# Kernel tuning notes

Measured on AMD Instinct MI355X. Metric: run time of the kernel, lower is better.

## Reference

```python
import jax, jax.numpy as jnp
import numpy as np

NUM_HEADS = 16
ROPE_BASE = 10000.0


def _rope_cos_sin(seq_len, head_dim, dtype):
    inv_freq = 1.0 / (ROPE_BASE ** (jnp.arange(0, head_dim, 2, dtype=jnp.float32) / head_dim))
    t = jnp.arange(seq_len, dtype=jnp.float32)
    freqs = t[:, None] * inv_freq[None, :]          # [S, hd/2]
    emb = jnp.concatenate([freqs, freqs], axis=-1)  # [S, hd]
    return jnp.cos(emb).astype(dtype), jnp.sin(emb).astype(dtype)


def _rotate_half(x):
    x1, x2 = jnp.split(x, 2, axis=-1)
    return jnp.concatenate([-x2, x1], axis=-1)


def setup_inputs() -> dict:
    key = jax.random.key(0)
    ks = jax.random.split(key, 5)
    B, S, D = 2, 2048, 2048
    x = jax.random.normal(ks[0], (B, S, D), dtype=jnp.float32)
    Wq = jax.random.normal(ks[1], (D, D), dtype=jnp.float32) * (D ** -0.5)
    Wk = jax.random.normal(ks[2], (D, D), dtype=jnp.float32) * (D ** -0.5)
    Wv = jax.random.normal(ks[3], (D, D), dtype=jnp.float32) * (D ** -0.5)
    Wo = jax.random.normal(ks[4], (D, D), dtype=jnp.float32) * (D ** -0.5)
    return {"x": x, "Wq": Wq, "Wk": Wk, "Wv": Wv, "Wo": Wo}


def reference(x, Wq, Wk, Wv, Wo):
    B, S, D = x.shape
    H = NUM_HEADS
    hd = D // H
    scale = hd ** -0.5
    # Linear(bias=False): y = x @ W.T ; reshape to [B, H, S, hd]
    def proj(W):
        return jnp.einsum('bsd,ed->bse', x, W).reshape(B, S, H, hd).transpose(0, 2, 1, 3)
    q, k, v = proj(Wq), proj(Wk), proj(Wv)
    cos, sin = _rope_cos_sin(S, hd, x.dtype)  # [S, hd]
    cos = cos[None, None, :, :]
    sin = sin[None, None, :, :]
    q = q * cos + _rotate_half(q) * sin
    k = k * cos + _rotate_half(k) * sin
    scores = jnp.einsum('bhqd,bhkd->bhqk', q, k) * scale  # [B,H,S,S]
    causal = jnp.triu(jnp.ones((S, S), dtype=bool), k=1)
    scores = jnp.where(causal[None, None], jnp.finfo(scores.dtype).min, scores)
    attn = jax.nn.softmax(scores, axis=-1)
    out = jnp.einsum('bhqk,bhkd->bhqd', attn, v)  # [B,H,S,hd]
    out = out.transpose(0, 2, 1, 3).reshape(B, S, D)
    return jnp.einsum('bsd,ed->bse', out, Wo)
```

## Files before the change

### kernel.cpp

```cpp
#include <hip/hip_runtime.h>
#include <hip/hip_bf16.h>
#include <math.h>

typedef __bf16 bf16_t;
typedef __attribute__((ext_vector_type(8))) __bf16 bf16x8;
typedef __attribute__((ext_vector_type(4))) float f32x4;

#define S_LEN 2048
#define DM    2048
#define NH    16
#define HD    128
#define MTOT  4096

__device__ inline float finz(float v) {
    return (v == v && fabsf(v) < 1e30f) ? v : 0.f;
}

__device__ inline void gload_lds16(const bf16_t* g, bf16_t* l) {
    __builtin_amdgcn_global_load_lds(
        (const __attribute__((address_space(1))) void*)g,
        (__attribute__((address_space(3))) void*)l, 16, 0, 0);
}

__global__ __launch_bounds__(256)
void dtype_probe(const unsigned short* __restrict__ p, unsigned int* __restrict__ flag)
{
    __shared__ int tot;
    if (threadIdx.x == 0) tot = 0;
    __syncthreads();
    int weird = 0;
    for (int i = threadIdx.x; i < 4096; i += 256) {
        unsigned short u = p[2*i];
        int e = (u >> 7) & 0xFF;
        if (e >= 0xC8 || (e != 0 && e <= 0x38)) weird++;
    }
    atomicAdd(&tot, weird);
    __syncthreads();
    if (threadIdx.x == 0) *flag = (tot > 512) ? 1u : 0u;
}

__global__ __launch_bounds__(256)
void convert_in(const void* __restrict__ src, bf16_t* __restrict__ dst, int n,
                const unsigned int* __restrict__ flag)
{
    const bool f32 = (*flag != 0);
    int i = (blockIdx.x*256 + threadIdx.x)*4;
    if (i + 3 >= n) return;
    if (f32) {
        const float4 v = *(const float4*)((const float*)src + i);
        dst[i  ] = (bf16_t)v.x; dst[i+1] = (bf16_t)v.y;
        dst[i+2] = (bf16_t)v.z; dst[i+3] = (bf16_t)v.w;
    } else {
        *(uint2*)(dst + i) = *(const uint2*)((const bf16_t*)src + i);
    }
}

template<int MODE>
__global__ __launch_bounds__(256)
void gemm_bt(const bf16_t* __restrict__ A, const bf16_t* __restrict__ W,
             void* __restrict__ Cv)
{
    __shared__ bf16_t As[128*64];
    __shared__ bf16_t Ws[128*64];

    const int t    = threadIdx.x;
    const int wv   = t >> 6;
    const int lane = t & 63;
    const int c16  = lane & 15;
    const int quad = lane >> 4;
    const int wm   = wv & 1;
    const int wn   = wv >> 1;
    const int mb   = blockIdx.x;
    const int nb   = blockIdx.y;
    const int c7   = c16 & 7;

    const int srow = lane >> 3;
    const int sphy = (lane & 7) ^ srow;
    const bf16_t* Ab = A + (size_t)(mb*128 + wv*32 + srow)*DM + sphy*8;
    const bf16_t* Wb = W + (size_t)(nb*128 + wv*32 + srow)*DM + sphy*8;

    f32x4 acc[4][4];
    #pragma unroll
    for (int i = 0; i < 4; ++i)
        #pragma unroll
        for (int j = 0; j < 4; ++j)
            acc[i][j] = (f32x4){0.f, 0.f, 0.f, 0.f};

    for (int kb = 0; kb < DM/64; ++kb) {
        __syncthreads();
        #pragma unroll
        for (int i = 0; i < 4; ++i) {
            gload_lds16(Ab + (size_t)kb*64 + (size_t)i*8*DM, As + (wv*32 + i*8)*64);
            gload_lds16(Wb + (size_t)kb*64 + (size_t)i*8*DM, Ws + (wv*32 + i*8)*64);
        }
        __syncthreads();

        #pragma unroll
        for (int kk = 0; kk < 2; ++kk) {
            const int ph = ((kk*4 + quad) ^ c7) * 8;
            bf16x8 af[4], bfr[4];
            #pragma unroll
            for (int mt = 0; mt < 4; ++mt)
                af[mt] = *(const bf16x8*)(As + (wm*64 + mt*16 + c16)*64 + ph);
            #pragma unroll
            for (int nt = 0; nt < 4; ++nt)
                bfr[nt] = *(const bf16x8*)(Ws + (nt*32 + wn*16 + c16)*64 + ph);
            #pragma unroll
            for (int mt = 0; mt < 4; ++mt)
                #pragma unroll
                for (int nt = 0; nt < 4; ++nt)
                    acc[mt][nt] = __builtin_amdgcn_mfma_f32_16x16x32_bf16(
                                      af[mt], bfr[nt], acc[mt][nt], 0, 0, 0);
        }
    }

    #pragma unroll
    for (int mt = 0; mt < 4; ++mt) {
        #pragma unroll
        for (int r = 0; r < 4; ++r) {
            const int m = mb*128 + wm*64 + mt*16 + quad*4 + r;
            if (MODE == 2) {
                bf16_t* C = (bf16_t*)Cv;
                size_t base = (size_t)m*DM + nb*128;
                #pragma unroll
                for (int nt = 0; nt < 4; ++nt)
                    C[base + nt*32 + wn*16 + c16] = (bf16_t)finz(acc[mt][nt][r]);
            } else if (MODE == 3) {
                float* C = (float*)Cv;
                size_t base = (size_t)m*DM + nb*128;
                #pragma unroll
                for (int nt = 0; nt < 4; ++nt)
                    C[base + nt*32 + wn*16 + c16] = finz(acc[mt][nt][r]);
            } else {
                bf16_t* C = (bf16_t*)Cv;
                const int b = m >> 11;
                const int s = m & (S_LEN - 1);
                size_t base = ((size_t)(b*NH + nb)*S_LEN + s)*HD;
                if (MODE == 1) {
                    #pragma unroll
                    for (int nt = 0; nt < 4; ++nt)
                        C[base + nt*32 + wn*16 + c16] = (bf16_t)finz(acc[mt][nt][r]);
                } else {
                    #pragma unroll
                    for (int nt = 0; nt < 2; ++nt) {
                        int t64 = nt*32 + wn*16 + c16;
                        float invf = exp2f(-(float)t64 * 0.20762050593046014f);
                        float ang  = (float)s * invf;
                        float sn, cs;
                        sincosf(ang, &sn, &cs);
                        float lo = acc[mt][nt  ][r];
                        float hi = acc[mt][nt+2][r];
                        C[base + t64     ] = (bf16_t)finz(lo*cs - hi*sn);
                        C[base + t64 + 64] = (bf16_t)finz(hi*cs + lo*sn);
                    }
                }
            }
        }
    }
}

__global__ __launch_bounds__(256)
void transpose_v(const bf16_t* __restrict__ Vb, bf16_t* __restrict__ VT)
{
    __shared__ bf16_t Lt[64*72];
    const int t  = threadIdx.x;
    const int st = blockIdx.x;
    const int dt = blockIdx.y;
    const int bh = blockIdx.z;
    #pragma unroll
    for (int i = 0; i < 2; ++i) {
        int ch = t + i*256;
        int sr = ch >> 3, c = ch & 7;
        *(uint4*)(Lt + sr*72 + c*8) =
            *(const uint4*)(Vb + ((size_t)bh*S_LEN + st*64 + sr)*HD + dt*64 + c*8);
    }
    __syncthreads();
    #pragma unroll
    for (int i = 0; i < 2; ++i) {
        int ch = t + i*256;
        int dr = ch >> 3, c = ch & 7;
        bf16x8 v;
        #pragma unroll
        for (int j = 0; j < 8; ++j) v[j] = Lt[(c*8 + j)*72 + dr];
        *(bf16x8*)(VT + ((size_t)bh*HD + dt*64 + dr)*S_LEN + st*64 + c*8) = v;
    }
}

__global__ __launch_bounds__(256)
void flash_attn(const bf16_t* __restrict__ Q, const bf16_t* __restrict__ K,
                const bf16_t* __restrict__ VT, bf16_t* __restrict__ O)
{
    __shared__ bf16_t Ks[64*128];
    __shared__ bf16_t Vs[128*64];
    __shared__ bf16_t Ps[4*16*64];

    const int t    = threadIdx.x;
    const int wv   = t >> 6;
    const int lane = t & 63;
    const int c16  = lane & 15;
    const int quad = lane >> 4;
    const int c7   = c16 & 7;
    const int ix   = blockIdx.x;
    const int bh   = blockIdx.y;

    const float scale = 0.08838834764831845f;
    const float SMAX  = 12.0f;

    bf16x8 onesf;
    #pragma unroll
    for (int j = 0; j < 8; ++j) onesf[j] = (bf16_t)1.0f;

    for (int pass = 0; pass < 2; ++pass) {
        const int qb = pass ? ix : 31 - ix;

        bf16x8 qf[4];
        {
            const size_t qbase = ((size_t)bh*S_LEN + qb*64 + wv*16 + c16)*HD;
            #pragma unroll
            for (int kk = 0; kk < 4; ++kk)
                qf[kk] = *(const bf16x8*)(Q + qbase + kk*32 + quad*8);
        }

        f32x4 oacc[8];
        #pragma unroll
        for (int i = 0; i < 8; ++i) oacc[i] = (f32x4){0.f, 0.f, 0.f, 0.f};
        f32x4 lacc = (f32x4){0.f, 0.f, 0.f, 0.f};

        for (int kt = 0; kt <= qb; ++kt) {
            __syncthreads();
            #pragma unroll
            for (int i = 0; i < 4; ++i) {
                int rg = wv*16 + i*4 + (lane >> 4);
                int ph = (lane & 15) ^ (rg & 7);
                gload_lds16(K + ((size_t)bh*S_LEN + kt*64 + rg)*HD + ph*8,
                            Ks + (wv*16 + i*4)*128);
            }
            #pragma unroll
            for (int i = 0; i < 4; ++i) {
                int dg = wv*32 + i*8 + (lane >> 3);
                int ph = (lane & 7) ^ (dg & 7);
                gload_lds16(VT + ((size_t)bh*HD + dg)*S_LEN + kt*64 + ph*8,
                            Vs + (wv*32 + i*8)*64);
            }
            __syncthreads();

            f32x4 sacc[4];
            #pragma unroll
            for (int i = 0; i < 4; ++i) sacc[i] = (f32x4){0.f, 0.f, 0.f, 0.f};
            #pragma unroll
            for (int kk = 0; kk < 4; ++kk) {
                const int ph = ((kk*4 + quad) ^ c7) * 8;
                #pragma unroll
                for (int nt = 0; nt < 4; ++nt) {
                    bf16x8 kf = *(const bf16x8*)(Ks + (nt*16 + c16)*128 + ph);
                    sacc[nt] = __builtin_amdgcn_mfma_f32_16x16x32_bf16(
                                   qf[kk], kf, sacc[nt], 0, 0, 0);
                }
            }

            float pv[4][4];
            if (kt == qb) {
                const int q0 = qb*64 + wv*16 + quad*4;
                #pragma unroll
                for (int nt = 0; nt < 4; ++nt) {
                    const int kg = kt*64 + nt*16 + c16;
                    #pragma unroll
                    for (int r = 0; r < 4; ++r)
                        pv[nt][r] = (kg <= q0 + r)
                                  ? __expf(sacc[nt][r]*scale - SMAX) : 0.f;
                }
            } else {
                #pragma unroll
                for (int nt = 0; nt < 4; ++nt)
                    #pragma unroll
                    for (int r = 0; r < 4; ++r)
                        pv[nt][r] = __expf(sacc[nt][r]*scale - SMAX);
            }

            #pragma unroll
            for (int nt = 0; nt < 4; ++nt) {
                #pragma unroll
                for (int r = 0; r < 4; ++r) {
                    int rp = quad*4 + r;
                    int pc = (nt*2 + (c16 >> 3)) ^ (rp & 7);
                    Ps[wv*1024 + rp*64 + pc*8 + c7] = (bf16_t)pv[nt][r];
                }
            }

            #pragma unroll
            for (int ks = 0; ks < 2; ++ks) {
                const int ph = ((ks*4 + quad) ^ c7) * 8;
                bf16x8 pf = *(const bf16x8*)(Ps + wv*1024 + c16*64 + ph);
                lacc = __builtin_amdgcn_mfma_f32_16x16x32_bf16(pf, onesf, lacc, 0, 0, 0);
                #pragma unroll
                for (int dt = 0; dt < 8; ++dt) {
                    bf16x8 vf = *(const bf16x8*)(Vs + (dt*16 + c16)*64 + ph);
                    oacc[dt] = __builtin_amdgcn_mfma_f32_16x16x32_bf16(
                                   pf, vf, oacc[dt], 0, 0, 0);
                }
            }
        }

        const int b = bh >> 4, h = bh & 15;
        #pragma unroll
        for (int dt = 0; dt < 8; ++dt) {
            #pragma unroll
            for (int r = 0; r < 4; ++r) {
                const int q = qb*64 + wv*16 + quad*4 + r;
                float rl = 1.0f / fmaxf(lacc[r], 1e-37f);
                O[((size_t)(b*S_LEN + q))*DM + h*HD + dt*16 + c16] =
                    (bf16_t)finz(oacc[dt][r] * rl);
            }
        }
    }
}

extern "C" void kernel_launch(void* const* d_in, const int* in_sizes, int n_in,
                              void* d_out, int out_size, void* d_ws, size_t ws_size,
                              hipStream_t stream)
{
    const void* x_raw  = d_in[0];
    const void* Wq_raw = d_in[1];
    const void* Wk_raw = d_in[2];
    const void* Wv_raw = d_in[3];
    const void* Wo_raw = d_in[4];

    const int NX = MTOT*DM;
    const int NW = DM*DM;

    unsigned int* flag = (unsigned int*)d_ws;
    bf16_t* xb  = (bf16_t*)((char*)d_ws + 16);
    bf16_t* Wqb = xb  + NX;
    bf16_t* Wkb = Wqb + NW;
    bf16_t* Wvb = Wkb + NW;
    bf16_t* Wob = Wvb + NW;
    bf16_t* Qb  = Wob + NW;
    bf16_t* Kb  = Qb + NX;
    bf16_t* Vb  = Kb + NX;
    bf16_t* Ob  = Vb + NX;
    bf16_t* VT  = xb;

    bool out_is_f32 = true;
    {
        void* base = nullptr; size_t sz = 0;
        if (hipMemGetAddressRange((hipDeviceptr_t*)&base, &sz,
                                  (hipDeviceptr_t)d_out) == hipSuccess && sz != 0) {
            if (sz < (size_t)out_size * 3) out_is_f32 = false;
        }
    }

    dim3 bb(256);
    hipLaunchKernelGGL(dtype_probe, dim3(1), bb, 0, stream,
                       (const unsigned short*)x_raw, flag);
    hipLaunchKernelGGL(convert_in, dim3(NX/1024), bb, 0, stream, x_raw,  xb,  NX, flag);
    hipLaunchKernelGGL(convert_in, dim3(NW/1024), bb, 0, stream, Wq_raw, Wqb, NW, flag);
    hipLaunchKernelGGL(convert_in, dim3(NW/1024), bb, 0, stream, Wk_raw, Wkb, NW, flag);
    hipLaunchKernelGGL(convert_in, dim3(NW/1024), bb, 0, stream, Wv_raw, Wvb, NW, flag);
    hipLaunchKernelGGL(convert_in, dim3(NW/1024), bb, 0, stream, Wo_raw, Wob, NW, flag);

    dim3 gg(32, 16);
    hipLaunchKernelGGL((gemm_bt<0>), gg, bb, 0, stream, xb, Wqb, (void*)Qb);
    hipLaunchKernelGGL((gemm_bt<0>), gg, bb, 0, stream, xb, Wkb, (void*)Kb);
    hipLaunchKernelGGL((gemm_bt<1>), gg, bb, 0, stream, xb, Wvb, (void*)Vb);
    hipLaunchKernelGGL(transpose_v, dim3(32, 2, 32), bb, 0, stream, Vb, VT);
    hipLaunchKernelGGL(flash_attn, dim3(16, 32), bb, 0, stream, Qb, Kb, VT, Ob);
    if (out_is_f32)
        hipLaunchKernelGGL((gemm_bt<3>), gg, bb, 0, stream, Ob, Wob, d_out);
    else
        hipLaunchKernelGGL((gemm_bt<2>), gg, bb, 0, stream, Ob, Wob, d_out);
}
```

Before: 449.2 us.

## Fuse QKV projections into one GEMM launch and restructure attention with 32x32 MFMA

Merges the three QKV projection GEMMs into a single launch with 48 column blocks, which relies on Wq/Wk/Wv and Qb/Kb/Vb being laid out contiguously in the workspace. The flash attention kernel now uses 512-thread blocks covering 128 query rows with 32x32x16 MFMAs. The key dimension is split across two wave groups whose partial outputs are combined through shared memory. P is repacked in registers with permlane32_swap instead of being round-tripped through LDS. Together these aim to cut launch count, LDS traffic and per-MFMA overhead, at the cost of more shared memory, a cross-wave reduction and reliance on the buffer layout.

```diff
diff --git a/kernel.cpp b/kernel.cpp
--- a/kernel.cpp
+++ b/kernel.cpp
@@ -5,6 +5,7 @@
 typedef __bf16 bf16_t;
 typedef __attribute__((ext_vector_type(8))) __bf16 bf16x8;
 typedef __attribute__((ext_vector_type(4))) float f32x4;
+typedef __attribute__((ext_vector_type(16))) float f32x16;
 
 #define S_LEN 2048
 #define DM    2048
@@ -21,6 +22,22 @@
         (const __attribute__((address_space(1))) void*)g,
         (__attribute__((address_space(3))) void*)l, 16, 0, 0);
 }
+
+__device__ __forceinline__ int crow4(int g, int hi) {
+    return (g & 3) + ((g >> 2) << 3) + (hi << 2);
+}
+__device__ __forceinline__ unsigned pk2(float x, float y) {
+    union { bf16_t h; unsigned short u; } a, b;
+    a.h = (bf16_t)x; b.h = (bf16_t)y;
+    return (unsigned)a.u | ((unsigned)b.u << 16);
+}
+__device__ __forceinline__ bf16x8 pack4(unsigned w0, unsigned w1, unsigned w2, unsigned w3) {
+    union { unsigned w[4]; bf16x8 v; } u;
+    u.w[0] = w0; u.w[1] = w1; u.w[2] = w2; u.w[3] = w3;
+    return u.v;
+}
+
+#define MFMA32(a, b, c) __builtin_amdgcn_mfma_f32_32x32x16_bf16(a, b, c, 0, 0, 0)
 
 __global__ __launch_bounds__(256)
 void dtype_probe(const unsigned short* __restrict__ p, unsigned int* __restrict__ flag)
@@ -132,11 +149,13 @@
                 for (int nt = 0; nt < 4; ++nt)
                     C[base + nt*32 + wn*16 + c16] = finz(acc[mt][nt][r]);
             } else {
-                bf16_t* C = (bf16_t*)Cv;
+                const int g  = nb >> 4;
+                const int hh = nb & 15;
+                bf16_t* C = (bf16_t*)Cv + (size_t)g * MTOT * DM;
                 const int b = m >> 11;
                 const int s = m & (S_LEN - 1);
-                size_t base = ((size_t)(b*NH + nb)*S_LEN + s)*HD;
-                if (MODE == 1) {
+                size_t base = ((size_t)(b*NH + hh)*S_LEN + s)*HD;
+                if (g == 2) {
                     #pragma unroll
                     for (int nt = 0; nt < 4; ++nt)
                         C[base + nt*32 + wn*16 + c16] = (bf16_t)finz(acc[mt][nt][r]);
@@ -148,10 +167,10 @@
                         float ang  = (float)s * invf;
                         float sn, cs;
                         sincosf(ang, &sn, &cs);
-                        float lo = acc[mt][nt  ][r];
-                        float hi = acc[mt][nt+2][r];
-                        C[base + t64     ] = (bf16_t)finz(lo*cs - hi*sn);
-                        C[base + t64 + 64] = (bf16_t)finz(hi*cs + lo*sn);
+                        float lo  = acc[mt][nt  ][r];
+                        float hi2 = acc[mt][nt+2][r];
+                        C[base + t64     ] = (bf16_t)finz(lo*cs - hi2*sn);
+                        C[base + t64 + 64] = (bf16_t)finz(hi2*cs + lo*sn);
                     }
                 }
             }
@@ -186,20 +205,22 @@
     }
 }
 
-__global__ __launch_bounds__(256)
+__global__ __launch_bounds__(512, 2)
 void flash_attn(const bf16_t* __restrict__ Q, const bf16_t* __restrict__ K,
                 const bf16_t* __restrict__ VT, bf16_t* __restrict__ O)
 {
     __shared__ bf16_t Ks[64*128];
     __shared__ bf16_t Vs[128*64];
-    __shared__ bf16_t Ps[4*16*64];
+    __shared__ float  Ocmb[4][32*128];
+    __shared__ float  lcmb[4][32];
 
     const int t    = threadIdx.x;
-    const int wv   = t >> 6;
+    const int wid  = t >> 6;
     const int lane = t & 63;
-    const int c16  = lane & 15;
-    const int quad = lane >> 4;
-    const int c7   = c16 & 7;
+    const int qw   = wid & 3;
+    const int kh   = wid >> 2;
+    const int c32  = lane & 31;
+    const int hi   = lane >> 5;
     const int ix   = blockIdx.x;
     const int bh   = blockIdx.y;
 
@@ -211,105 +232,130 @@
     for (int j = 0; j < 8; ++j) onesf[j] = (bf16_t)1.0f;
 
     for (int pass = 0; pass < 2; ++pass) {
-        const int qb = pass ? ix : 31 - ix;
-
-        bf16x8 qf[4];
+        const int Qt   = pass ? (15 - ix) : ix;
+        const int qt0  = Qt * 128;
+        const int qrow = qt0 + qw*32 + c32;
+        const int qmin = qt0 + qw*32;
+
+        bf16x8 qf[8];
         {
-            const size_t qbase = ((size_t)bh*S_LEN + qb*64 + wv*16 + c16)*HD;
-            #pragma unroll
-            for (int kk = 0; kk < 4; ++kk)
-                qf[kk] = *(const bf16x8*)(Q + qbase + kk*32 + quad*8);
-        }
-
-        f32x4 oacc[8];
-        #pragma unroll
-        for (int i = 0; i < 8; ++i) oacc[i] = (f32x4){0.f, 0.f, 0.f, 0.f};
-        f32x4 lacc = (f32x4){0.f, 0.f, 0.f, 0.f};
-
-        for (int kt = 0; kt <= qb; ++kt) {
+            const bf16_t* qp = Q + ((size_t)bh*S_LEN + qrow)*HD;
+            #pragma unroll
+            for (int s = 0; s < 8; ++s)
+                qf[s] = *(const bf16x8*)(qp + s*16 + hi*8);
+        }
+
+        f32x16 oacc[4];
+        f32x16 lacc;
+        #pragma unroll
+        for (int e = 0; e < 16; ++e) lacc[e] = 0.f;
+        #pragma unroll
+        for (int dt = 0; dt < 4; ++dt)
+            #pragma unroll
+            for (int e = 0; e < 16; ++e) oacc[dt][e] = 0.f;
+
+        const int ktend = 2*Qt + 1;
+        for (int kt = 0; kt <= ktend; ++kt) {
             __syncthreads();
             #pragma unroll
-            for (int i = 0; i < 4; ++i) {
-                int rg = wv*16 + i*4 + (lane >> 4);
-                int ph = (lane & 15) ^ (rg & 7);
+            for (int j = 0; j < 2; ++j) {
+                int base = wid*8 + j*4;
+                int rg   = base + (lane >> 4);
+                int ph   = (lane & 15) ^ (rg & 7);
                 gload_lds16(K + ((size_t)bh*S_LEN + kt*64 + rg)*HD + ph*8,
-                            Ks + (wv*16 + i*4)*128);
-            }
-            #pragma unroll
-            for (int i = 0; i < 4; ++i) {
-                int dg = wv*32 + i*8 + (lane >> 3);
-                int ph = (lane & 7) ^ (dg & 7);
-                gload_lds16(VT + ((size_t)bh*HD + dg)*S_LEN + kt*64 + ph*8,
-                            Vs + (wv*32 + i*8)*64);
+                            Ks + base*128);
+            }
+            #pragma unroll
+            for (int j = 0; j < 2; ++j) {
+                int base = wid*16 + j*8;
+                int rg   = base + (lane >> 3);
+                int ph   = (lane & 7) ^ (rg & 7);
+                gload_lds16(VT + ((size_t)bh*HD + rg)*S_LEN + kt*64 + ph*8,
+                            Vs + base*64);
             }
             __syncthreads();
 
-            f32x4 sacc[4];
-            #pragma unroll
-            for (int i = 0; i < 4; ++i) sacc[i] = (f32x4){0.f, 0.f, 0.f, 0.f};
-            #pragma unroll
-            for (int kk = 0; kk < 4; ++kk) {
-                const int ph = ((kk*4 + quad) ^ c7) * 8;
-                #pragma unroll
-                for (int nt = 0; nt < 4; ++nt) {
-                    bf16x8 kf = *(const bf16x8*)(Ks + (nt*16 + c16)*128 + ph);
-                    sacc[nt] = __builtin_amdgcn_mfma_f32_16x16x32_bf16(
-                                   qf[kk], kf, sacc[nt], 0, 0, 0);
-                }
-            }
-
-            float pv[4][4];
-            if (kt == qb) {
-                const int q0 = qb*64 + wv*16 + quad*4;
-                #pragma unroll
-                for (int nt = 0; nt < 4; ++nt) {
-                    const int kg = kt*64 + nt*16 + c16;
-                    #pragma unroll
-                    for (int r = 0; r < 4; ++r)
-                        pv[nt][r] = (kg <= q0 + r)
-                                  ? __expf(sacc[nt][r]*scale - SMAX) : 0.f;
+            const int kbase = kt*64 + kh*32;
+            if (kbase > qmin + 31) continue;
+
+            f32x16 sacc;
+            #pragma unroll
+            for (int e = 0; e < 16; ++e) sacc[e] = 0.f;
+            const int krow = kh*32 + c32;
+            const int ksw  = krow & 7;
+            #pragma unroll
+            for (int s = 0; s < 8; ++s) {
+                bf16x8 kf = *(const bf16x8*)(Ks + krow*128 + (((s*2 + hi) ^ ksw) << 3));
+                sacc = MFMA32(kf, qf[s], sacc);
+            }
+
+            float p[16];
+            if (kbase + 31 > qmin) {
+                #pragma unroll
+                for (int g = 0; g < 16; ++g) {
+                    int kg = kbase + crow4(g, hi);
+                    p[g] = (kg <= qrow) ? __expf(sacc[g]*scale - SMAX) : 0.f;
                 }
             } else {
                 #pragma unroll
-                for (int nt = 0; nt < 4; ++nt)
-                    #pragma unroll
-                    for (int r = 0; r < 4; ++r)
-                        pv[nt][r] = __expf(sacc[nt][r]*scale - SMAX);
-            }
-
-            #pragma unroll
-            for (int nt = 0; nt < 4; ++nt) {
-                #pragma unroll
-                for (int r = 0; r < 4; ++r) {
-                    int rp = quad*4 + r;
-                    int pc = (nt*2 + (c16 >> 3)) ^ (rp & 7);
-                    Ps[wv*1024 + rp*64 + pc*8 + c7] = (bf16_t)pv[nt][r];
+                for (int g = 0; g < 16; ++g)
+                    p[g] = __expf(sacc[g]*scale - SMAX);
+            }
+
+            unsigned a0 = pk2(p[0],  p[1]),  b0 = pk2(p[2],  p[3]);
+            unsigned a1 = pk2(p[4],  p[5]),  b1 = pk2(p[6],  p[7]);
+            unsigned a2 = pk2(p[8],  p[9]),  b2 = pk2(p[10], p[11]);
+            unsigned a3 = pk2(p[12], p[13]), b3 = pk2(p[14], p[15]);
+            asm volatile("v_permlane32_swap_b32 %0, %1" : "+v"(a0), "+v"(a1));
+            asm volatile("v_permlane32_swap_b32 %0, %1" : "+v"(b0), "+v"(b1));
+            asm volatile("v_permlane32_swap_b32 %0, %1" : "+v"(a2), "+v"(a3));
+            asm volatile("v_permlane32_swap_b32 %0, %1" : "+v"(b2), "+v"(b3));
+            bf16x8 pa0 = pack4(a0, b0, a1, b1);
+            bf16x8 pa1 = pack4(a2, b2, a3, b3);
+
+            lacc = MFMA32(pa0, onesf, lacc);
+            lacc = MFMA32(pa1, onesf, lacc);
+            const int ks0 = kh*2 + 0, ks1 = kh*2 + 1;
+            #pragma unroll
+            for (int dt = 0; dt < 4; ++dt) {
+                const int vrow = dt*32 + c32;
+                const int vsw  = vrow & 7;
+                bf16x8 vf0 = *(const bf16x8*)(Vs + vrow*64 + (((ks0*2 + hi) ^ vsw) << 3));
+                oacc[dt] = MFMA32(pa0, vf0, oacc[dt]);
+                bf16x8 vf1 = *(const bf16x8*)(Vs + vrow*64 + (((ks1*2 + hi) ^ vsw) << 3));
+                oacc[dt] = MFMA32(pa1, vf1, oacc[dt]);
+            }
+        }
+
+        if (kh == 1) {
+            #pragma unroll
+            for (int g = 0; g < 16; ++g) {
+                int ql = crow4(g, hi);
+                #pragma unroll
+                for (int dt = 0; dt < 4; ++dt)
+                    Ocmb[qw][ql*128 + dt*32 + c32] = oacc[dt][g];
+            }
+            if (c32 == 0) {
+                #pragma unroll
+                for (int g = 0; g < 16; ++g)
+                    lcmb[qw][crow4(g, hi)] = lacc[g];
+            }
+        }
+        __syncthreads();
+        if (kh == 0) {
+            const int b = bh >> 4, h = bh & 15;
+            #pragma unroll
+            for (int g = 0; g < 16; ++g) {
+                int ql = crow4(g, hi);
+                int qg = qt0 + qw*32 + ql;
+                float lt = lacc[g] + lcmb[qw][ql];
+                float rl = 1.0f / fmaxf(lt, 1e-37f);
+                #pragma unroll
+                for (int dt = 0; dt < 4; ++dt) {
+                    float v = oacc[dt][g] + Ocmb[qw][ql*128 + dt*32 + c32];
+                    O[((size_t)(b*S_LEN + qg))*DM + h*HD + dt*32 + c32] =
+                        (bf16_t)finz(v*rl);
                 }
-            }
-
-            #pragma unroll
-            for (int ks = 0; ks < 2; ++ks) {
-                const int ph = ((ks*4 + quad) ^ c7) * 8;
-                bf16x8 pf = *(const bf16x8*)(Ps + wv*1024 + c16*64 + ph);
-                lacc = __builtin_amdgcn_mfma_f32_16x16x32_bf16(pf, onesf, lacc, 0, 0, 0);
-                #pragma unroll
-                for (int dt = 0; dt < 8; ++dt) {
-                    bf16x8 vf = *(const bf16x8*)(Vs + (dt*16 + c16)*64 + ph);
-                    oacc[dt] = __builtin_amdgcn_mfma_f32_16x16x32_bf16(
-                                   pf, vf, oacc[dt], 0, 0, 0);
-                }
-            }
-        }
-
-        const int b = bh >> 4, h = bh & 15;
-        #pragma unroll
-        for (int dt = 0; dt < 8; ++dt) {
-            #pragma unroll
-            for (int r = 0; r < 4; ++r) {
-                const int q = qb*64 + wv*16 + quad*4 + r;
-                float rl = 1.0f / fmaxf(lacc[r], 1e-37f);
-                O[((size_t)(b*S_LEN + q))*DM + h*HD + dt*16 + c16] =
-                    (bf16_t)finz(oacc[dt][r] * rl);
             }
         }
     }
@@ -358,14 +404,11 @@
     hipLaunchKernelGGL(convert_in, dim3(NW/1024), bb, 0, stream, Wv_raw, Wvb, NW, flag);
     hipLaunchKernelGGL(convert_in, dim3(NW/1024), bb, 0, stream, Wo_raw, Wob, NW, flag);
 
-    dim3 gg(32, 16);
-    hipLaunchKernelGGL((gemm_bt<0>), gg, bb, 0, stream, xb, Wqb, (void*)Qb);
-    hipLaunchKernelGGL((gemm_bt<0>), gg, bb, 0, stream, xb, Wkb, (void*)Kb);
-    hipLaunchKernelGGL((gemm_bt<1>), gg, bb, 0, stream, xb, Wvb, (void*)Vb);
+    hipLaunchKernelGGL((gemm_bt<4>), dim3(32, 48), bb, 0, stream, xb, Wqb, (void*)Qb);
     hipLaunchKernelGGL(transpose_v, dim3(32, 2, 32), bb, 0, stream, Vb, VT);
-    hipLaunchKernelGGL(flash_attn, dim3(16, 32), bb, 0, stream, Qb, Kb, VT, Ob);
+    hipLaunchKernelGGL(flash_attn, dim3(8, 32), dim3(512), 0, stream, Qb, Kb, VT, Ob);
     if (out_is_f32)
-        hipLaunchKernelGGL((gemm_bt<3>), gg, bb, 0, stream, Ob, Wob, d_out);
+        hipLaunchKernelGGL((gemm_bt<3>), dim3(32, 16), bb, 0, stream, Ob, Wob, d_out);
     else
-        hipLaunchKernelGGL((gemm_bt<2>), gg, bb, 0, stream, Ob, Wob, d_out);
-}
+        hipLaunchKernelGGL((gemm_bt<2>), dim3(32, 16), bb, 0, stream, Ob, Wob, d_out);
+}
```

New measurement: 417.9 us. 1.07x faster.
